# Kernel tuning notes

Hardware: AMD Instinct MI355X
Metric: run time of the kernel (lower is better)

Reference implementation:

```python
import jax, jax.numpy as jnp
import numpy as np

MIN_SIGMA = 0.001


def setup_inputs() -> dict:
    key = jax.random.key(0)
    kA, kB = jax.random.split(key)
    A = jax.random.normal(kA, (8, 2048, 128), dtype=jnp.float32)
    B = jax.random.normal(kB, (4096, 128), dtype=jnp.float32)
    sigma = jnp.float32(1.0)
    return {"A": A, "B": B, "sigma": sigma}


def reference(A, B, sigma):
    # A: (bs, n, d), B: (m, d) -> K: (bs, n, m)
    A_norm = jnp.sum(A * A, axis=-1, keepdims=True)          # (bs, n, 1)
    B_norm = jnp.sum(B * B, axis=-1)[None, None, :]          # (1, 1, m)
    AB = jnp.einsum('bnd,md->bnm', A, B)                     # (bs, n, m)
    dist2 = jnp.maximum(A_norm + B_norm - 2.0 * AB, 0.0)
    sig = jnp.maximum(sigma, MIN_SIGMA)
    K = jnp.exp(-dist2 / (2.0 * sig * sig))
    return K
```

## Files before the change

kernel.cpp:

```cpp
#include <hip/hip_runtime.h>


typedef __attribute__((ext_vector_type(8))) short bf16x8;
typedef __attribute__((ext_vector_type(4))) float f32x4;

#define NROW_A 16384
#define NROW_B 4096
#define D      128

#define OFF_AHI 0u
#define OFF_BHI (OFF_AHI + NROW_A * D * 2u)
#define OFF_NA  (OFF_BHI + NROW_B * D * 2u)
#define OFF_NB  (OFF_NA + NROW_A * 4u)
#define WS_NEED (OFF_NB + NROW_B * 4u)

__device__ __forceinline__ short f2bf_hi(float x) {
    union { float f; unsigned u; } v; v.f = x;
    unsigned r = (v.u + 0x7fffu + ((v.u >> 16) & 1u)) >> 16;
    return (short)r;
}
__device__ __forceinline__ float bf2f(short h) {
    union { unsigned u; float f; } v; v.u = ((unsigned)(unsigned short)h) << 16;
    return v.f;
}

__global__ __launch_bounds__(256)
void rbf_precompute(const float* __restrict__ A, const float* __restrict__ Bm,
                    short* __restrict__ Ahi, short* __restrict__ Bhi,
                    float* __restrict__ nA, float* __restrict__ nB) {
    const int g   = blockIdx.x * 256 + threadIdx.x;
    const int row = g >> 4;
    const int c   = g & 15;

    const float* src; short* dhi; float* nrm; int r;
    if (row < NROW_A) {
        r = row; src = A + (size_t)r * D;
        dhi = Ahi + (size_t)r * D; nrm = nA + r;
    } else {
        r = row - NROW_A; src = Bm + (size_t)r * D;
        dhi = Bhi + (size_t)r * D; nrm = nB + r;
    }

    float4 v0 = *(const float4*)(src + c * 8);
    float4 v1 = *(const float4*)(src + c * 8 + 4);
    float f[8] = {v0.x, v0.y, v0.z, v0.w, v1.x, v1.y, v1.z, v1.w};

    bf16x8 hi;
    float ss = 0.0f;
#pragma unroll
    for (int e = 0; e < 8; ++e) {
        hi[e] = f2bf_hi(f[e]);
        ss += f[e] * f[e];
    }
    *(bf16x8*)(dhi + c * 8) = hi;

#pragma unroll
    for (int m = 1; m <= 8; m <<= 1) ss += __shfl_xor(ss, m);
    if (c == 0) *nrm = ss;
}

__global__ __launch_bounds__(512, 4)
void rbf_mfma_persist(const short* __restrict__ Ahi, const short* __restrict__ Bhi,
                      const float* __restrict__ nAg, const float* __restrict__ nBg,
                      const float* __restrict__ sigp, float* __restrict__ out) {
    __shared__ __align__(16) short sA[128 * 128];
    __shared__ __align__(16) short sB[128 * 128];
    __shared__ __align__(16) float snA[128];
    __shared__ __align__(16) float snB[128];

    const int tid = threadIdx.x;
    const int bid = blockIdx.x;
    const int xcd = bid & 7;
    const int idx = bid >> 3;
    const int bcol = ((xcd << 2) + (idx & 3)) << 7;
    const int bg   = idx >> 2;

    const int srow = tid >> 2;
    const int sc4  = tid & 3;

#pragma unroll
    for (int it = 0; it < 4; ++it) {
        const int c  = sc4 + (it << 2);
        const int cs = c ^ (srow & 15);
        *(bf16x8*)&sB[srow * 128 + cs * 8] =
            *(const bf16x8*)&Bhi[(size_t)(bcol + srow) * D + c * 8];
    }
    if (tid < 128) snB[tid] = nBg[bcol + tid];

    {
        const int brow0 = (bg << 3) << 7;
#pragma unroll
        for (int it = 0; it < 4; ++it) {
            const int c  = sc4 + (it << 2);
            const int cs = c ^ (srow & 15);
            *(bf16x8*)&sA[srow * 128 + cs * 8] =
                *(const bf16x8*)&Ahi[(size_t)(brow0 + srow) * D + c * 8];
        }
        if (tid >= 384) snA[tid - 384] = nAg[brow0 + tid - 384];
    }
    __syncthreads();

    const int lane = tid & 63;
    const int w    = tid >> 6;
    const int wr   = (w >> 1) << 5;
    const int wc   = (w & 1) << 6;
    const int lr   = lane & 15;
    const int kb   = lane >> 4;

    float sg = fmaxf(sigp[0], 0.001f);
    const float cc = -0.5f / (sg * sg);

    bf16x8 rh[4];
    float rn = 0.0f;

    for (int t = 0; t < 8; ++t) {
        const int browt = ((bg << 3) + t) << 7;

        if (t < 7) {
            const int brn = browt + 128;
#pragma unroll
            for (int it = 0; it < 4; ++it) {
                const int c = sc4 + (it << 2);
                rh[it] = *(const bf16x8*)&Ahi[(size_t)(brn + srow) * D + c * 8];
            }
            if (tid >= 384) rn = nAg[brn + tid - 384];
        }

        f32x4 acc[2][4] = {};
#pragma unroll
        for (int ks = 0; ks < 4; ++ks) {
            const int off = (((ks << 2) + kb) ^ lr) << 3;
            bf16x8 af[2], bf[4];
#pragma unroll
            for (int i = 0; i < 2; ++i)
                af[i] = *(const bf16x8*)&sA[(wr + (i << 4) + lr) * 128 + off];
#pragma unroll
            for (int j = 0; j < 4; ++j)
                bf[j] = *(const bf16x8*)&sB[(wc + (j << 4) + lr) * 128 + off];
#pragma unroll
            for (int i = 0; i < 2; ++i)
#pragma unroll
                for (int j = 0; j < 4; ++j)
                    acc[i][j] = __builtin_amdgcn_mfma_f32_16x16x32_bf16(bf[j], af[i], acc[i][j], 0, 0, 0);
        }

#pragma unroll
        for (int i = 0; i < 2; ++i) {
            const int orow = wr + (i << 4) + lr;
            const float na = snA[orow];
#pragma unroll
            for (int j = 0; j < 4; ++j) {
                const int ocol = wc + (j << 4) + (kb << 2);
                const f32x4 nb = *(const f32x4*)&snB[ocol];
                f32x4 v;
#pragma unroll
                for (int r = 0; r < 4; ++r) {
                    float d2 = fmaxf(na + nb[r] - 2.0f * acc[i][j][r], 0.0f);
                    v[r] = __expf(d2 * cc);
                }
                *(f32x4*)(out + (size_t)(browt + orow) * 4096 + bcol + ocol) = v;
            }
        }

        __syncthreads();

        if (t < 7) {
#pragma unroll
            for (int it = 0; it < 4; ++it) {
                const int c  = sc4 + (it << 2);
                const int cs = c ^ (srow & 15);
                *(bf16x8*)&sA[srow * 128 + cs * 8] = rh[it];
            }
            if (tid >= 384) snA[tid - 384] = rn;
            __syncthreads();
        }
    }
}

#define PK 136
__global__ __launch_bounds__(256, 2)
void rbf_mfma_fallback(const float* __restrict__ A, const float* __restrict__ Bm,
                       const float* __restrict__ sigp, float* __restrict__ out) {
    __shared__ __align__(16) short sAhi[64 * PK];
    __shared__ __align__(16) short sAlo[64 * PK];
    __shared__ __align__(16) short sBhi[64 * PK];
    __shared__ __align__(16) short sBlo[64 * PK];
    __shared__ float nA[64];
    __shared__ float nB[64];

    const int tid  = threadIdx.x;
    const int brow = blockIdx.y << 6;
    const int bcol = blockIdx.x << 6;

    const int r0 = tid >> 5;
    const int kq = (tid & 31) << 2;
#pragma unroll
    for (int it = 0; it < 8; ++it) {
        const int row = r0 + (it << 3);
        const float4 va = *(const float4*)(A  + (size_t)(brow + row) * 128 + kq);
        const float4 vb = *(const float4*)(Bm + (size_t)(bcol + row) * 128 + kq);
        short4 ha, la, hb, lb;
        ha.x = f2bf_hi(va.x); la.x = f2bf_hi(va.x - bf2f(ha.x));
        ha.y = f2bf_hi(va.y); la.y = f2bf_hi(va.y - bf2f(ha.y));
        ha.z = f2bf_hi(va.z); la.z = f2bf_hi(va.z - bf2f(ha.z));
        ha.w = f2bf_hi(va.w); la.w = f2bf_hi(va.w - bf2f(ha.w));
        hb.x = f2bf_hi(vb.x); lb.x = f2bf_hi(vb.x - bf2f(hb.x));
        hb.y = f2bf_hi(vb.y); lb.y = f2bf_hi(vb.y - bf2f(hb.y));
        hb.z = f2bf_hi(vb.z); lb.z = f2bf_hi(vb.z - bf2f(hb.z));
        hb.w = f2bf_hi(vb.w); lb.w = f2bf_hi(vb.w - bf2f(hb.w));
        const int idx = row * PK + kq;
        *(short4*)(&sAhi[idx]) = ha;
        *(short4*)(&sAlo[idx]) = la;
        *(short4*)(&sBhi[idx]) = hb;
        *(short4*)(&sBlo[idx]) = lb;
        float sa = va.x * va.x + va.y * va.y + va.z * va.z + va.w * va.w;
        float sb = vb.x * vb.x + vb.y * vb.y + vb.z * vb.z + vb.w * vb.w;
#pragma unroll
        for (int m = 16; m >= 1; m >>= 1) { sa += __shfl_xor(sa, m); sb += __shfl_xor(sb, m); }
        if ((tid & 31) == 0) { nA[row] = sa; nB[row] = sb; }
    }
    __syncthreads();

    const int lane = tid & 63;
    const int w    = tid >> 6;
    const int wr   = (w >> 1) << 5;
    const int wc   = (w & 1) << 5;
    const int lr   = lane & 15;
    const int kb   = lane >> 4;
    f32x4 acc[2][2] = {};
#pragma unroll
    for (int ks = 0; ks < 4; ++ks) {
        const int kc = (ks << 5) + (kb << 3);
        bf16x8 ahi[2], alo[2], bhi[2], blo[2];
#pragma unroll
        for (int i = 0; i < 2; ++i) {
            const int ar = (wr + (i << 4) + lr) * PK + kc;
            ahi[i] = *(const bf16x8*)(&sAhi[ar]);
            alo[i] = *(const bf16x8*)(&sAlo[ar]);
            const int br = (wc + (i << 4) + lr) * PK + kc;
            bhi[i] = *(const bf16x8*)(&sBhi[br]);
            blo[i] = *(const bf16x8*)(&sBlo[br]);
        }
#pragma unroll
        for (int i = 0; i < 2; ++i)
#pragma unroll
            for (int j = 0; j < 2; ++j) {
                acc[i][j] = __builtin_amdgcn_mfma_f32_16x16x32_bf16(ahi[i], bhi[j], acc[i][j], 0, 0, 0);
                acc[i][j] = __builtin_amdgcn_mfma_f32_16x16x32_bf16(ahi[i], blo[j], acc[i][j], 0, 0, 0);
                acc[i][j] = __builtin_amdgcn_mfma_f32_16x16x32_bf16(alo[i], bhi[j], acc[i][j], 0, 0, 0);
            }
    }
    float sg = fmaxf(sigp[0], 0.001f);
    const float c = -0.5f / (sg * sg);
#pragma unroll
    for (int i = 0; i < 2; ++i)
#pragma unroll
        for (int j = 0; j < 2; ++j)
#pragma unroll
            for (int r = 0; r < 4; ++r) {
                const int lrow = wr + (i << 4) + (kb << 2) + r;
                const int lcol = wc + (j << 4) + lr;
                float d2 = nA[lrow] + nB[lcol] - 2.0f * acc[i][j][r];
                d2 = fmaxf(d2, 0.0f);
                out[(size_t)(brow + lrow) * 4096 + (bcol + lcol)] = __expf(d2 * c);
            }
}

extern "C" void kernel_launch(void* const* d_in, const int* in_sizes, int n_in,
                              void* d_out, int out_size, void* d_ws, size_t ws_size,
                              hipStream_t stream) {
    const float* A    = (const float*)d_in[0];
    const float* Bm   = (const float*)d_in[1];
    const float* sigp = (const float*)d_in[2];
    float* out = (float*)d_out;

    if (ws_size >= WS_NEED) {
        char* ws = (char*)d_ws;
        short* Ahi = (short*)(ws + OFF_AHI);
        short* Bhi = (short*)(ws + OFF_BHI);
        float* nA  = (float*)(ws + OFF_NA);
        float* nB  = (float*)(ws + OFF_NB);

        dim3 pgrid((NROW_A + NROW_B) * 16 / 256, 1, 1);
        rbf_precompute<<<pgrid, 256, 0, stream>>>(A, Bm, Ahi, Bhi, nA, nB);

        rbf_mfma_persist<<<dim3(512, 1, 1), dim3(512, 1, 1), 0, stream>>>(
            Ahi, Bhi, nA, nB, sigp, out);
    } else {
        dim3 grid(4096 / 64, 16384 / 64, 1);
        rbf_mfma_fallback<<<grid, dim3(256, 1, 1), 0, stream>>>(A, Bm, sigp, out);
    }
}
```

Before: 60.11 us.

## Drop LDS staging; load MFMA fragments directly from global memory

Replaces the LDS-staged persistent kernel with a streaming kernel that reads bf16 A and B fragments for each MFMA straight from global memory. Blocks shrink to 256 threads over 64-row tiles, the grid doubles to 1024, and the B norms are held in registers. This removes shared-memory writes and __syncthreads barriers, but it gives up cross-wave reuse through LDS and depends on L1/L2 caching for the repeated fragment reads.

```diff
diff --git a/kernel.cpp b/kernel.cpp
--- a/kernel.cpp
+++ b/kernel.cpp
@@ -59,46 +59,15 @@
     if (c == 0) *nrm = ss;
 }
 
-__global__ __launch_bounds__(512, 4)
-void rbf_mfma_persist(const short* __restrict__ Ahi, const short* __restrict__ Bhi,
-                      const float* __restrict__ nAg, const float* __restrict__ nBg,
-                      const float* __restrict__ sigp, float* __restrict__ out) {
-    __shared__ __align__(16) short sA[128 * 128];
-    __shared__ __align__(16) short sB[128 * 128];
-    __shared__ __align__(16) float snA[128];
-    __shared__ __align__(16) float snB[128];
-
+__global__ __launch_bounds__(256, 4)
+void rbf_mfma_stream(const short* __restrict__ Ahi, const short* __restrict__ Bhi,
+                     const float* __restrict__ nAg, const float* __restrict__ nBg,
+                     const float* __restrict__ sigp, float* __restrict__ out) {
     const int tid = threadIdx.x;
     const int bid = blockIdx.x;
     const int xcd = bid & 7;
-    const int idx = bid >> 3;
-    const int bcol = ((xcd << 2) + (idx & 3)) << 7;
-    const int bg   = idx >> 2;
-
-    const int srow = tid >> 2;
-    const int sc4  = tid & 3;
-
-#pragma unroll
-    for (int it = 0; it < 4; ++it) {
-        const int c  = sc4 + (it << 2);
-        const int cs = c ^ (srow & 15);
-        *(bf16x8*)&sB[srow * 128 + cs * 8] =
-            *(const bf16x8*)&Bhi[(size_t)(bcol + srow) * D + c * 8];
-    }
-    if (tid < 128) snB[tid] = nBg[bcol + tid];
-
-    {
-        const int brow0 = (bg << 3) << 7;
-#pragma unroll
-        for (int it = 0; it < 4; ++it) {
-            const int c  = sc4 + (it << 2);
-            const int cs = c ^ (srow & 15);
-            *(bf16x8*)&sA[srow * 128 + cs * 8] =
-                *(const bf16x8*)&Ahi[(size_t)(brow0 + srow) * D + c * 8];
-        }
-        if (tid >= 384) snA[tid - 384] = nAg[brow0 + tid - 384];
-    }
-    __syncthreads();
+    const int bcol = ((xcd << 2) + ((bid >> 3) & 3)) << 7;
+    const int bg   = bid >> 5;
 
     const int lane = tid & 63;
     const int w    = tid >> 6;
@@ -110,33 +79,25 @@
     float sg = fmaxf(sigp[0], 0.001f);
     const float cc = -0.5f / (sg * sg);
 
-    bf16x8 rh[4];
-    float rn = 0.0f;
+    f32x4 nb[4];
+#pragma unroll
+    for (int j = 0; j < 4; ++j)
+        nb[j] = *(const f32x4*)&nBg[bcol + wc + (j << 4) + (kb << 2)];
 
     for (int t = 0; t < 8; ++t) {
-        const int browt = ((bg << 3) + t) << 7;
-
-        if (t < 7) {
-            const int brn = browt + 128;
-#pragma unroll
-            for (int it = 0; it < 4; ++it) {
-                const int c = sc4 + (it << 2);
-                rh[it] = *(const bf16x8*)&Ahi[(size_t)(brn + srow) * D + c * 8];
-            }
-            if (tid >= 384) rn = nAg[brn + tid - 384];
-        }
+        const int browt = ((bg << 3) + t) << 6;
 
         f32x4 acc[2][4] = {};
 #pragma unroll
         for (int ks = 0; ks < 4; ++ks) {
-            const int off = (((ks << 2) + kb) ^ lr) << 3;
+            const int koff = ((ks << 2) + kb) << 3;
             bf16x8 af[2], bf[4];
 #pragma unroll
             for (int i = 0; i < 2; ++i)
-                af[i] = *(const bf16x8*)&sA[(wr + (i << 4) + lr) * 128 + off];
+                af[i] = *(const bf16x8*)&Ahi[(size_t)(browt + wr + (i << 4) + lr) * D + koff];
 #pragma unroll
             for (int j = 0; j < 4; ++j)
-                bf[j] = *(const bf16x8*)&sB[(wc + (j << 4) + lr) * 128 + off];
+                bf[j] = *(const bf16x8*)&Bhi[(size_t)(bcol + wc + (j << 4) + lr) * D + koff];
 #pragma unroll
             for (int i = 0; i < 2; ++i)
 #pragma unroll
@@ -146,33 +107,18 @@
 
 #pragma unroll
         for (int i = 0; i < 2; ++i) {
-            const int orow = wr + (i << 4) + lr;
-            const float na = snA[orow];
+            const int orow = browt + wr + (i << 4) + lr;
+            const float na = nAg[orow];
 #pragma unroll
             for (int j = 0; j < 4; ++j) {
-                const int ocol = wc + (j << 4) + (kb << 2);
-                const f32x4 nb = *(const f32x4*)&snB[ocol];
                 f32x4 v;
 #pragma unroll
                 for (int r = 0; r < 4; ++r) {
-                    float d2 = fmaxf(na + nb[r] - 2.0f * acc[i][j][r], 0.0f);
+                    float d2 = fmaxf(na + nb[j][r] - 2.0f * acc[i][j][r], 0.0f);
                     v[r] = __expf(d2 * cc);
                 }
-                *(f32x4*)(out + (size_t)(browt + orow) * 4096 + bcol + ocol) = v;
+                *(f32x4*)(out + (size_t)orow * 4096 + bcol + wc + (j << 4) + (kb << 2)) = v;
             }
-        }
-
-        __syncthreads();
-
-        if (t < 7) {
-#pragma unroll
-            for (int it = 0; it < 4; ++it) {
-                const int c  = sc4 + (it << 2);
-                const int cs = c ^ (srow & 15);
-                *(bf16x8*)&sA[srow * 128 + cs * 8] = rh[it];
-            }
-            if (tid >= 384) snA[tid - 384] = rn;
-            __syncthreads();
         }
     }
 }
@@ -284,7 +230,7 @@
         dim3 pgrid((NROW_A + NROW_B) * 16 / 256, 1, 1);
         rbf_precompute<<<pgrid, 256, 0, stream>>>(A, Bm, Ahi, Bhi, nA, nB);
 
-        rbf_mfma_persist<<<dim3(512, 1, 1), dim3(512, 1, 1), 0, stream>>>(
+        rbf_mfma_stream<<<dim3(1024, 1, 1), dim3(256, 1, 1), 0, stream>>>(
             Ahi, Bhi, nA, nB, sigp, out);
     } else {
         dim3 grid(4096 / 64, 16384 / 64, 1);
```

After: 89.02 us. +48.1%, slower.
